# Kernel optimization log

Hardware: AMD Instinct MI355X
Metric: run time of the kernel (lower is better)

Reference implementation:

```python
import jax, jax.numpy as jnp
import numpy as np

X_SCALE, X_ZP = 0.03, -66      # int8 quant params (qmin=-128, qmax=127)
Y_SCALE, Y_ZP = 0.025, 160     # uint8 quant params (qmin=0, qmax=255)
M = K = N = 4096


def setup_inputs() -> dict:
    key = jax.random.key(0)
    kx, ky = jax.random.split(key)
    # x holds int8-range values [-128, 127], y holds uint8-range values [0, 255]
    x = jax.random.randint(kx, (M, K), -128, 128, dtype=jnp.int32)
    y = jax.random.randint(ky, (K, N), 0, 256, dtype=jnp.int32)
    return {"x": x, "y": y}


def reference(x, y):
    # dequantize_per_tensor: (q - zero_point) * scale  (values already in [qmin, qmax])
    xf = (x.astype(jnp.float32) - X_ZP) * X_SCALE   # [M, K]
    yf = (y.astype(jnp.float32) - Y_ZP) * Y_SCALE   # [K, N]
    return jnp.matmul(xf, yf)                       # [M, N]
```

## Files before the change

kernel.cpp:

```cpp
#include <hip/hip_runtime.h>
#include <stdint.h>

#define Mdim 4096
#define Kdim 4096
#define Ndim 4096

typedef __attribute__((ext_vector_type(4))) int v4i;
typedef __attribute__((ext_vector_type(16))) int v16i;

__device__ __forceinline__ void gload_lds16(const void* g, void* l) {
  __builtin_amdgcn_global_load_lds(
      (__attribute__((address_space(1))) void*)(uintptr_t)g,
      (__attribute__((address_space(3))) void*)(uint32_t)(uintptr_t)l,
      16, 0, 0);
}

__global__ __launch_bounds__(256) void pack_x_kernel(const int* __restrict__ x,
                                                     char* __restrict__ x8,
                                                     int* __restrict__ rsx) {
  const int row = blockIdx.x;
  const int t = threadIdx.x;
  const int4* src = (const int4*)(x + (size_t)row * Kdim);
  int* dst = (int*)(x8 + (size_t)row * Kdim);
  int sum = 0;
#pragma unroll
  for (int i = 0; i < 4; ++i) {
    int4 v = src[t + 256 * i];
    sum += v.x + v.y + v.z + v.w;
    dst[t + 256 * i] =
        (v.x & 0xff) | ((v.y & 0xff) << 8) | ((v.z & 0xff) << 16) | (v.w << 24);
  }
#pragma unroll
  for (int o = 32; o > 0; o >>= 1) sum += __shfl_down(sum, o, 64);
  __shared__ int red[4];
  if ((t & 63) == 0) red[t >> 6] = sum;
  __syncthreads();
  if (t == 0) rsx[row] = red[0] + red[1] + red[2] + red[3];
}

__global__ __launch_bounds__(256) void pack_yt_kernel(const int* __restrict__ y,
                                                      char* __restrict__ yt,
                                                      int* __restrict__ csy) {
  __shared__ int wt[64 * 17];
  const int t = threadIdx.x;
  const int n0 = blockIdx.x * 64;
  const int k0 = blockIdx.y * 64;
  const int c = t & 15;
  const int r0 = t >> 4;
#pragma unroll
  for (int s = 0; s < 4; ++s) {
    const int r = r0 + s * 16;
    int4 v = *(const int4*)(y + (size_t)(k0 + r) * Ndim + n0 + c * 4);
    v.x -= 128; v.y -= 128; v.z -= 128; v.w -= 128;
    wt[r * 17 + c] =
        (v.x & 0xff) | ((v.y & 0xff) << 8) | ((v.z & 0xff) << 16) | (v.w << 24);
  }
  __syncthreads();
  const int n = t >> 2;
  const int kq = t & 3;
  const int colw = n >> 2;
  const int byi = (n & 3) * 8;
  int outw[4];
  int bsum = 0;
#pragma unroll
  for (int j = 0; j < 4; ++j) {
    int b[4];
#pragma unroll
    for (int jj = 0; jj < 4; ++jj) {
      const int word = wt[(kq * 16 + j * 4 + jj) * 17 + colw];
      b[jj] = (word >> byi) & 0xff;
      bsum += (int)(char)b[jj];
    }
    outw[j] = b[0] | (b[1] << 8) | (b[2] << 16) | (b[3] << 24);
  }
  *(int4*)(yt + (size_t)(n0 + n) * Kdim + k0 + kq * 16) =
      make_int4(outw[0], outw[1], outw[2], outw[3]);
  bsum += __shfl_xor(bsum, 1, 64);
  bsum += __shfl_xor(bsum, 2, 64);
  if (kq == 0) atomicAdd(csy + n0 + n, bsum);
}

__global__ __launch_bounds__(512, 2) void gemm_i8_kernel(
    const char* __restrict__ A, const char* __restrict__ B,
    const int* __restrict__ rsx, const int* __restrict__ csy,
    float* __restrict__ out) {
  __shared__ __align__(16) char lds[3 * 32768];
  const int t = threadIdx.x;
  const int l = t & 63;
  const int w = t >> 6;
  const int warow = w >> 1;
  const int wbcol = w & 1;
  const int bm = blockIdx.y * 256;
  const int bn = blockIdx.x * 256;

  v16i acc[2][4];
#pragma unroll
  for (int i = 0; i < 2; ++i)
#pragma unroll
    for (int j = 0; j < 4; ++j)
#pragma unroll
      for (int q = 0; q < 16; ++q) acc[i][j][q] = 0;

  const int srow = t >> 2;
  const int cswz = ((t & 3) ^ ((t >> 3) & 3)) * 16;
  const char* gA = A + (size_t)(bm + srow) * Kdim + cswz;
  const char* gB = B + (size_t)(bn + srow) * Kdim + cswz;

#define STAGE(buf_off, koff)                                                  \
  do {                                                                        \
    _Pragma("unroll") for (int i = 0; i < 2; ++i)                             \
        gload_lds16(gA + (koff) + (size_t)i * 128 * Kdim,                     \
                    lds + (buf_off) + i * 8192 + t * 16);                     \
    _Pragma("unroll") for (int i = 0; i < 2; ++i)                             \
        gload_lds16(gB + (koff) + (size_t)i * 128 * Kdim,                     \
                    lds + (buf_off) + 16384 + i * 8192 + t * 16);             \
  } while (0)

  const int arow = warow * 64 + (l & 31);
  const int brow = wbcol * 128 + (l & 31);
  const int lhalf = l >> 5;
  const int lkey = (l >> 1) & 3;

#define COMPUTE(buf_off)                                                      \
  do {                                                                        \
    const char* As = lds + (buf_off);                                         \
    const char* Bs = lds + (buf_off) + 16384;                                 \
    __builtin_amdgcn_s_setprio(1);                                            \
    _Pragma("unroll") for (int ks = 0; ks < 2; ++ks) {                        \
      const int slot = ((ks * 2 + lhalf) ^ lkey) * 16;                        \
      v4i a[2], b[4];                                                         \
      _Pragma("unroll") for (int i = 0; i < 2; ++i)                           \
          a[i] = *(const v4i*)(As + (arow + i * 32) * 64 + slot);             \
      _Pragma("unroll") for (int j = 0; j < 4; ++j)                           \
          b[j] = *(const v4i*)(Bs + (brow + j * 32) * 64 + slot);             \
      _Pragma("unroll") for (int i = 0; i < 2; ++i)                           \
          _Pragma("unroll") for (int j = 0; j < 4; ++j)                       \
              acc[i][j] = __builtin_amdgcn_mfma_i32_32x32x32_i8(              \
                  a[i], b[j], acc[i][j], 0, 0, 0);                            \
    }                                                                         \
    __builtin_amdgcn_s_setprio(0);                                            \
  } while (0)

#define BAR()                                                                 \
  do {                                                                        \
    asm volatile("" ::: "memory");                                            \
    __builtin_amdgcn_s_barrier();                                             \
    asm volatile("" ::: "memory");                                            \
  } while (0)
#define WAITV(n) asm volatile("s_waitcnt vmcnt(" #n ")" ::: "memory")

  STAGE(0, 0);
  STAGE(32768, 1 * 64);
  STAGE(65536, 2 * 64);
  WAITV(8);
  BAR();

#pragma unroll 1
  for (int kt = 0; kt < 60; kt += 3) {
    COMPUTE(0);
    BAR();
    STAGE(0, (kt + 3) * 64);
    WAITV(8);
    BAR();
    COMPUTE(32768);
    BAR();
    STAGE(32768, (kt + 4) * 64);
    WAITV(8);
    BAR();
    COMPUTE(65536);
    BAR();
    STAGE(65536, (kt + 5) * 64);
    WAITV(8);
    BAR();
  }
  COMPUTE(0);
  BAR();
  STAGE(0, 63 * 64);
  WAITV(8);
  BAR();
  COMPUTE(32768);
  BAR();
  WAITV(4);
  BAR();
  COMPUTE(65536);
  BAR();
  WAITV(0);
  BAR();
  COMPUTE(0);

  const int col = l & 31;
#pragma unroll
  for (int i = 0; i < 2; ++i) {
    const int gm0 = bm + warow * 64 + i * 32;
#pragma unroll
    for (int j = 0; j < 4; ++j) {
      const int gn = bn + wbcol * 128 + j * 32 + col;
      const int cs = 66 * csy[gn] - 8650752;
#pragma unroll
      for (int r = 0; r < 16; ++r) {
        const int row = (r & 3) + 8 * (r >> 2) + 4 * lhalf;
        const int gm = gm0 + row;
        const int val = acc[i][j][r] - 32 * rsx[gm] + cs;
        out[(size_t)gm * Ndim + gn] = 7.5e-4f * (float)val;
      }
    }
  }
#undef STAGE
#undef COMPUTE
#undef BAR
#undef WAITV
}

extern "C" void kernel_launch(void* const* d_in, const int* in_sizes, int n_in,
                              void* d_out, int out_size, void* d_ws, size_t ws_size,
                              hipStream_t stream) {
  (void)in_sizes; (void)n_in; (void)out_size; (void)ws_size;
  const int* x = (const int*)d_in[0];
  const int* y = (const int*)d_in[1];
  float* out = (float*)d_out;
  char* ws = (char*)d_ws;
  char* x8 = ws;
  char* yt = ws + (size_t)Mdim * Kdim;
  int* rsx = (int*)(ws + (size_t)Mdim * Kdim + (size_t)Kdim * Ndim);
  int* csy = rsx + Mdim;

  hipMemsetAsync(csy, 0, Ndim * sizeof(int), stream);
  pack_x_kernel<<<Mdim, 256, 0, stream>>>(x, x8, rsx);
  pack_yt_kernel<<<dim3(Ndim / 64, Kdim / 64), 256, 0, stream>>>(y, yt, csy);
  gemm_i8_kernel<<<dim3(Ndim / 256, Mdim / 256), 512, 0, stream>>>(x8, yt, rsx, csy, out);
}
```

Baseline: 243.4 us.

## Fuse packing kernels, drop memset/atomics, shrink GEMM tile to 128x256

Combines the x and y packing kernels into one launch. Column blocks now each own 16 columns across the full K range, so column sums are written directly without the memset and atomics. The GEMM block shrinks from 256x256 with 512 threads to 128x256 with 256 threads, giving 512 blocks instead of 256 to fill the CUs better. The cost is less tile reuse of B per block. The y-pack blocks loop serially over K with only 256 blocks, which may lengthen that phase.

```diff
diff --git a/kernel.cpp b/kernel.cpp
--- a/kernel.cpp
+++ b/kernel.cpp
@@ -15,82 +15,90 @@
       16, 0, 0);
 }
 
-__global__ __launch_bounds__(256) void pack_x_kernel(const int* __restrict__ x,
-                                                     char* __restrict__ x8,
-                                                     int* __restrict__ rsx) {
-  const int row = blockIdx.x;
+__global__ __launch_bounds__(512) void pack_fused_kernel(
+    const int* __restrict__ x, const int* __restrict__ y,
+    char* __restrict__ x8, char* __restrict__ yt, int* __restrict__ rsx,
+    int* __restrict__ csy) {
+  __shared__ int shm[512 * 5];
   const int t = threadIdx.x;
-  const int4* src = (const int4*)(x + (size_t)row * Kdim);
-  int* dst = (int*)(x8 + (size_t)row * Kdim);
-  int sum = 0;
-#pragma unroll
-  for (int i = 0; i < 4; ++i) {
-    int4 v = src[t + 256 * i];
-    sum += v.x + v.y + v.z + v.w;
-    dst[t + 256 * i] =
-        (v.x & 0xff) | ((v.y & 0xff) << 8) | ((v.z & 0xff) << 16) | (v.w << 24);
+  if (blockIdx.x < 256) {
+    const int n0 = blockIdx.x * 16;
+    const int n = t >> 5;
+    const int kq = t & 31;
+    const int colw = n >> 2;
+    const int byi = (n & 3) * 8;
+    int bsum = 0;
+#pragma unroll 1
+    for (int c = 0; c < 8; ++c) {
+      const int k0 = c * 512;
+#pragma unroll
+      for (int p = 0; p < 4; ++p) {
+        const int r = (t >> 2) + p * 128;
+        int4 v = *(const int4*)(y + (size_t)(k0 + r) * Ndim + n0 + (t & 3) * 4);
+        int wd = (v.x & 0xff) | ((v.y & 0xff) << 8) | ((v.z & 0xff) << 16) |
+                 (v.w << 24);
+        shm[r * 5 + (t & 3)] = wd ^ 0x80808080;
+      }
+      __syncthreads();
+      int outw[4];
+#pragma unroll
+      for (int j = 0; j < 4; ++j) {
+        int b[4];
+#pragma unroll
+        for (int jj = 0; jj < 4; ++jj) {
+          const int word = shm[(kq * 16 + j * 4 + jj) * 5 + colw];
+          b[jj] = (word >> byi) & 0xff;
+          bsum += (int)(char)b[jj];
+        }
+        outw[j] = b[0] | (b[1] << 8) | (b[2] << 16) | (b[3] << 24);
+      }
+      *(int4*)(yt + (size_t)(n0 + n) * Kdim + k0 + kq * 16) =
+          make_int4(outw[0], outw[1], outw[2], outw[3]);
+      __syncthreads();
+    }
+    bsum += __shfl_xor(bsum, 1, 64);
+    bsum += __shfl_xor(bsum, 2, 64);
+    bsum += __shfl_xor(bsum, 4, 64);
+    bsum += __shfl_xor(bsum, 8, 64);
+    bsum += __shfl_xor(bsum, 16, 64);
+    if (kq == 0) csy[n0 + n] = bsum;
+  } else {
+    const int rowp = (int)(blockIdx.x - 256) * 2;
+    const int h = t >> 8;
+    const int tt = t & 255;
+    const int row = rowp + h;
+    const int4* src = (const int4*)(x + (size_t)row * Kdim);
+    int4* dst = (int4*)(x8 + (size_t)row * Kdim);
+    int sum = 0;
+    int wd[4];
+#pragma unroll
+    for (int i = 0; i < 4; ++i) {
+      int4 v = src[tt * 4 + i];
+      sum += v.x + v.y + v.z + v.w;
+      wd[i] = (v.x & 0xff) | ((v.y & 0xff) << 8) | ((v.z & 0xff) << 16) |
+              (v.w << 24);
+    }
+    dst[tt] = make_int4(wd[0], wd[1], wd[2], wd[3]);
+#pragma unroll
+    for (int o = 32; o > 0; o >>= 1) sum += __shfl_down(sum, o, 64);
+    if ((t & 63) == 0) shm[t >> 6] = sum;
+    __syncthreads();
+    if (t == 0) rsx[rowp] = shm[0] + shm[1] + shm[2] + shm[3];
+    if (t == 256) rsx[rowp + 1] = shm[4] + shm[5] + shm[6] + shm[7];
   }
-#pragma unroll
-  for (int o = 32; o > 0; o >>= 1) sum += __shfl_down(sum, o, 64);
-  __shared__ int red[4];
-  if ((t & 63) == 0) red[t >> 6] = sum;
-  __syncthreads();
-  if (t == 0) rsx[row] = red[0] + red[1] + red[2] + red[3];
-}
-
-__global__ __launch_bounds__(256) void pack_yt_kernel(const int* __restrict__ y,
-                                                      char* __restrict__ yt,
-                                                      int* __restrict__ csy) {
-  __shared__ int wt[64 * 17];
-  const int t = threadIdx.x;
-  const int n0 = blockIdx.x * 64;
-  const int k0 = blockIdx.y * 64;
-  const int c = t & 15;
-  const int r0 = t >> 4;
-#pragma unroll
-  for (int s = 0; s < 4; ++s) {
-    const int r = r0 + s * 16;
-    int4 v = *(const int4*)(y + (size_t)(k0 + r) * Ndim + n0 + c * 4);
-    v.x -= 128; v.y -= 128; v.z -= 128; v.w -= 128;
-    wt[r * 17 + c] =
-        (v.x & 0xff) | ((v.y & 0xff) << 8) | ((v.z & 0xff) << 16) | (v.w << 24);
-  }
-  __syncthreads();
-  const int n = t >> 2;
-  const int kq = t & 3;
-  const int colw = n >> 2;
-  const int byi = (n & 3) * 8;
-  int outw[4];
-  int bsum = 0;
-#pragma unroll
-  for (int j = 0; j < 4; ++j) {
-    int b[4];
-#pragma unroll
-    for (int jj = 0; jj < 4; ++jj) {
-      const int word = wt[(kq * 16 + j * 4 + jj) * 17 + colw];
-      b[jj] = (word >> byi) & 0xff;
-      bsum += (int)(char)b[jj];
-    }
-    outw[j] = b[0] | (b[1] << 8) | (b[2] << 16) | (b[3] << 24);
-  }
-  *(int4*)(yt + (size_t)(n0 + n) * Kdim + k0 + kq * 16) =
-      make_int4(outw[0], outw[1], outw[2], outw[3]);
-  bsum += __shfl_xor(bsum, 1, 64);
-  bsum += __shfl_xor(bsum, 2, 64);
-  if (kq == 0) atomicAdd(csy + n0 + n, bsum);
-}
-
-__global__ __launch_bounds__(512, 2) void gemm_i8_kernel(
+}
+
+__global__ __launch_bounds__(256, 2) void gemm_i8_kernel(
     const char* __restrict__ A, const char* __restrict__ B,
     const int* __restrict__ rsx, const int* __restrict__ csy,
     float* __restrict__ out) {
-  __shared__ __align__(16) char lds[3 * 32768];
+  __shared__ __align__(16) char lds[3 * 24576];
   const int t = threadIdx.x;
   const int l = t & 63;
   const int w = t >> 6;
   const int warow = w >> 1;
   const int wbcol = w & 1;
-  const int bm = blockIdx.y * 256;
+  const int bm = blockIdx.y * 128;
   const int bn = blockIdx.x * 256;
 
   v16i acc[2][4];
@@ -109,11 +117,11 @@
 #define STAGE(buf_off, koff)                                                  \
   do {                                                                        \
     _Pragma("unroll") for (int i = 0; i < 2; ++i)                             \
-        gload_lds16(gA + (koff) + (size_t)i * 128 * Kdim,                     \
-                    lds + (buf_off) + i * 8192 + t * 16);                     \
-    _Pragma("unroll") for (int i = 0; i < 2; ++i)                             \
-        gload_lds16(gB + (koff) + (size_t)i * 128 * Kdim,                     \
-                    lds + (buf_off) + 16384 + i * 8192 + t * 16);             \
+        gload_lds16(gA + (koff) + (size_t)i * 64 * Kdim,                      \
+                    lds + (buf_off) + i * 4096 + t * 16);                     \
+    _Pragma("unroll") for (int i = 0; i < 4; ++i)                             \
+        gload_lds16(gB + (koff) + (size_t)i * 64 * Kdim,                      \
+                    lds + (buf_off) + 8192 + i * 4096 + t * 16);              \
   } while (0)
 
   const int arow = warow * 64 + (l & 31);
@@ -121,11 +129,21 @@
   const int lhalf = l >> 5;
   const int lkey = (l >> 1) & 3;
 
+#define MFMA(a, b, c) __builtin_amdgcn_mfma_i32_32x32x32_i8(a, b, c, 0, 0, 0)
+#define SETP(n) __builtin_amdgcn_s_setprio(n)
+#define BAR()                                                                 \
+  do {                                                                        \
+    asm volatile("" ::: "memory");                                            \
+    __builtin_amdgcn_s_barrier();                                             \
+    asm volatile("" ::: "memory");                                            \
+  } while (0)
+#define WAITV(n) asm volatile("s_waitcnt vmcnt(" #n ")" ::: "memory")
+
 #define COMPUTE(buf_off)                                                      \
   do {                                                                        \
     const char* As = lds + (buf_off);                                         \
-    const char* Bs = lds + (buf_off) + 16384;                                 \
-    __builtin_amdgcn_s_setprio(1);                                            \
+    const char* Bs = lds + (buf_off) + 8192;                                  \
+    SETP(1);                                                                  \
     _Pragma("unroll") for (int ks = 0; ks < 2; ++ks) {                        \
       const int slot = ((ks * 2 + lhalf) ^ lkey) * 16;                        \
       v4i a[2], b[4];                                                         \
@@ -135,24 +153,15 @@
           b[j] = *(const v4i*)(Bs + (brow + j * 32) * 64 + slot);             \
       _Pragma("unroll") for (int i = 0; i < 2; ++i)                           \
           _Pragma("unroll") for (int j = 0; j < 4; ++j)                       \
-              acc[i][j] = __builtin_amdgcn_mfma_i32_32x32x32_i8(              \
-                  a[i], b[j], acc[i][j], 0, 0, 0);                            \
+              acc[i][j] = MFMA(a[i], b[j], acc[i][j]);                        \
     }                                                                         \
-    __builtin_amdgcn_s_setprio(0);                                            \
+    SETP(0);                                                                  \
   } while (0)
 
-#define BAR()                                                                 \
-  do {                                                                        \
-    asm volatile("" ::: "memory");                                            \
-    __builtin_amdgcn_s_barrier();                                             \
-    asm volatile("" ::: "memory");                                            \
-  } while (0)
-#define WAITV(n) asm volatile("s_waitcnt vmcnt(" #n ")" ::: "memory")
-
   STAGE(0, 0);
-  STAGE(32768, 1 * 64);
-  STAGE(65536, 2 * 64);
-  WAITV(8);
+  STAGE(24576, 64);
+  STAGE(49152, 128);
+  WAITV(12);
   BAR();
 
 #pragma unroll 1
@@ -160,29 +169,29 @@
     COMPUTE(0);
     BAR();
     STAGE(0, (kt + 3) * 64);
-    WAITV(8);
-    BAR();
-    COMPUTE(32768);
-    BAR();
-    STAGE(32768, (kt + 4) * 64);
-    WAITV(8);
-    BAR();
-    COMPUTE(65536);
-    BAR();
-    STAGE(65536, (kt + 5) * 64);
-    WAITV(8);
+    WAITV(12);
+    BAR();
+    COMPUTE(24576);
+    BAR();
+    STAGE(24576, (kt + 4) * 64);
+    WAITV(12);
+    BAR();
+    COMPUTE(49152);
+    BAR();
+    STAGE(49152, (kt + 5) * 64);
+    WAITV(12);
     BAR();
   }
   COMPUTE(0);
   BAR();
   STAGE(0, 63 * 64);
-  WAITV(8);
-  BAR();
-  COMPUTE(32768);
-  BAR();
-  WAITV(4);
-  BAR();
-  COMPUTE(65536);
+  WAITV(12);
+  BAR();
+  COMPUTE(24576);
+  BAR();
+  WAITV(6);
+  BAR();
+  COMPUTE(49152);
   BAR();
   WAITV(0);
   BAR();
@@ -207,6 +216,8 @@
   }
 #undef STAGE
 #undef COMPUTE
+#undef MFMA
+#undef SETP
 #undef BAR
 #undef WAITV
 }
@@ -224,8 +235,7 @@
   int* rsx = (int*)(ws + (size_t)Mdim * Kdim + (size_t)Kdim * Ndim);
   int* csy = rsx + Mdim;
 
-  hipMemsetAsync(csy, 0, Ndim * sizeof(int), stream);
-  pack_x_kernel<<<Mdim, 256, 0, stream>>>(x, x8, rsx);
-  pack_yt_kernel<<<dim3(Ndim / 64, Kdim / 64), 256, 0, stream>>>(y, yt, csy);
-  gemm_i8_kernel<<<dim3(Ndim / 256, Mdim / 256), 512, 0, stream>>>(x8, yt, rsx, csy, out);
-}
+  pack_fused_kernel<<<256 + Mdim / 2, 512, 0, stream>>>(x, y, x8, yt, rsx, csy);
+  gemm_i8_kernel<<<dim3(Ndim / 256, Mdim / 128), 256, 0, stream>>>(x8, yt, rsx,
+                                                                   csy, out);
+}
```

New measurement: 251.9 us. 3.5% more time.
